# Kernel tuning notes

Hardware: AMD Instinct MI355X
Metric: run time of the kernel (lower is better)

The kernel has to match this reference:

```python
import jax, jax.numpy as jnp
import numpy as np

N_NODES = 6890
N_ANGLES = 8
K_CHEB = 15
N_DESC = 544
HIDDEN = 64
N_CLASS = 6890
M = N_ANGLES * N_NODES  # 55120, size of anisotropic Laplacian
DEG = 16
NNZ = M * DEG
BN_EPS = 1e-5


def setup_inputs() -> dict:
    key = jax.random.key(0)
    ks = jax.random.split(key, 16)
    x = jax.random.normal(ks[0], (N_NODES, N_DESC), dtype=jnp.float32)
    # sparse anisotropic Laplacian (M x M), ~DEG nnz per row
    rows = jnp.repeat(jnp.arange(M, dtype=jnp.int32), DEG)
    cols = jax.random.randint(ks[1], (NNZ,), 0, M, dtype=jnp.int32)
    vals = jax.random.normal(ks[2], (NNZ,), dtype=jnp.float32) * 0.1
    # conv1: (K, n_angles*n_desc, 64); conv2..6 stacked: (5, K, n_angles*64, 64)
    def xavier(k, shape, fan_in, fan_out):
        lim = np.sqrt(6.0 / (fan_in + fan_out))
        return jax.random.uniform(k, shape, jnp.float32, -lim, lim)
    W1 = xavier(ks[3], (K_CHEB, N_ANGLES * N_DESC, HIDDEN), N_ANGLES * N_DESC, HIDDEN)
    Wc = xavier(ks[4], (5, K_CHEB, N_ANGLES * HIDDEN, HIDDEN), N_ANGLES * HIDDEN, HIDDEN)
    conv_b = jnp.zeros((6, HIDDEN), jnp.float32)
    bn_gamma = jnp.ones((6, HIDDEN), jnp.float32)
    bn_beta = jnp.zeros((6, HIDDEN), jnp.float32)
    fc2_w = xavier(ks[5], (HIDDEN, 256), HIDDEN, 256)
    fc2_b = jnp.zeros((256,), jnp.float32)
    fc3_w = xavier(ks[6], (256, N_CLASS), 256, N_CLASS)
    fc3_b = jnp.zeros((N_CLASS,), jnp.float32)
    return {"x": x, "rows": rows, "cols": cols, "vals": vals,
            "W1": W1, "Wc": Wc, "conv_b": conv_b,
            "bn_gamma": bn_gamma, "bn_beta": bn_beta,
            "fc2_w": fc2_w, "fc2_b": fc2_b, "fc3_w": fc3_w, "fc3_b": fc3_b}


def _spmm(rows, cols, vals, T):
    # (M x M sparse) @ (M x C) via gather + segment-sum
    return jax.ops.segment_sum(vals[:, None] * T[cols], rows, num_segments=M)


def _acs_conv(x, rows, cols, vals, W, b):
    # x: (N, C). Chebyshev recurrence on the (A*N, C) angle-stacked signal.
    N, C = x.shape
    A = N_ANGLES

    def proj(T, Wk):
        # (A*N, C) -> (N, A*C) @ (A*C, out)
        return T.reshape(A, N, C).transpose(1, 0, 2).reshape(N, A * C) @ Wk

    T0 = jnp.tile(x, (A, 1))
    out = proj(T0, W[0])
    T1 = _spmm(rows, cols, vals, T0)
    out = out + proj(T1, W[1])
    for k in range(2, K_CHEB):
        T2 = 2.0 * _spmm(rows, cols, vals, T1) - T0
        out = out + proj(T2, W[k])
        T0, T1 = T1, T2
    return out + b


def _bn_relu(x, gamma, beta):
    # BatchNorm1d (training-mode batch stats, biased variance) + ReLU
    mean = jnp.mean(x, axis=0)
    var = jnp.var(x, axis=0)
    return jax.nn.relu((x - mean) * jax.lax.rsqrt(var + BN_EPS) * gamma + beta)


def reference(x, rows, cols, vals, W1, Wc, conv_b, bn_gamma, bn_beta,
              fc2_w, fc2_b, fc3_w, fc3_b):
    h = _bn_relu(_acs_conv(x, rows, cols, vals, W1, conv_b[0]), bn_gamma[0], bn_beta[0])
    for i in range(5):
        h = _bn_relu(_acs_conv(h, rows, cols, vals, Wc[i], conv_b[i + 1]),
                     bn_gamma[i + 1], bn_beta[i + 1])
    h = jax.nn.relu(h @ fc2_w + fc2_b)
    # dropout is identity at inference
    return h @ fc3_w + fc3_b
```

## Files before the change

kernel.cpp:

```cpp
#include <hip/hip_runtime.h>
#include <cstdint>
#include <cstddef>

#define NN 6890
#define NA 8
#define KC 15
#define ND 544
#define MR (NA * NN)
#define DEG 16
#define NNZ (MR * DEG)
#define BN_EPS 1e-5f
#define NRG 108
#define PB (NA * NRG)

typedef unsigned int u32;
typedef _Float16 f16;
typedef __attribute__((ext_vector_type(8))) _Float16 f16x8;
typedef __attribute__((ext_vector_type(4))) float f32x4;

union U4H8 { uint4 q; f16 h[8]; f16x8 v; };

__device__ __forceinline__ u32 packh(float a, float b) {
    union { f16 h[2]; u32 u; } c;
    c.h[0] = (f16)a; c.h[1] = (f16)b; return c.u;
}
__device__ __forceinline__ uint4 pack8h(const float* t) {
    uint4 m;
    m.x = packh(t[0], t[1]); m.y = packh(t[2], t[3]);
    m.z = packh(t[4], t[5]); m.w = packh(t[6], t[7]);
    return m;
}
__device__ __forceinline__ void acc8h(float* s, float v, uint4 g) {
    U4H8 c; c.q = g;
    #pragma unroll
    for (int i = 0; i < 8; ++i) s[i] += v * (float)c.h[i];
}

__global__ __launch_bounds__(256)
void prep_cv_kernel(const int* __restrict__ cols, const float* __restrict__ vals,
                    uint4* __restrict__ cvq)
{
    const int q = blockIdx.x * 256 + threadIdx.x;
    if (q >= NNZ / 4) return;
    const int4   c = ((const int4*)cols)[q];
    const float4 v = ((const float4*)vals)[q];
    uint4 o;
    o.x = ((u32)c.x & 0xffffu) | ((u32)c.y << 16);
    o.y = ((u32)c.z & 0xffffu) | ((u32)c.w << 16);
    o.z = packh(v.x, v.y);
    o.w = packh(v.z, v.w);
    cvq[q] = o;
}

template<int CC>
__global__ __launch_bounds__(256)
void tile_slab_kernel(const float* __restrict__ X, int C_in, int c0,
                      uint4* __restrict__ slab0)
{
    constexpr int LPR = CC / 8;
    constexpr int RPB = 256 / LPR;
    const int tid = threadIdx.x;
    const int j = tid % LPR, rloc = tid / LPR;
    const int r = blockIdx.x * RPB + rloc;
    if (r >= MR) return;
    const int n = r % NN;
    const float* xp = X + (size_t)n * C_in + c0 + 8 * j;
    const float4 t0 = *(const float4*)xp;
    const float4 t1 = *(const float4*)(xp + 4);
    float t[8] = { t0.x, t0.y, t0.z, t0.w, t1.x, t1.y, t1.z, t1.w };
    slab0[(size_t)r * LPR + j] = pack8h(t);
}

template<int CC, bool CHEB>
__device__ __forceinline__
void spmm_body(const uint4* __restrict__ sp, const uint4* __restrict__ sc,
               uint4* __restrict__ sw, const uint4* __restrict__ cvq)
{
    constexpr int LPR = CC / 8;
    constexpr int RPB = 256 / LPR;
    const int tid = threadIdx.x;
    const int j = tid % LPR, rloc = tid / LPR;
    const int r = blockIdx.x * RPB + rloc;
    if (r >= MR) return;

    int c[16]; float v[16];
    const uint4* cvp = cvq + (size_t)r * 4;
    #pragma unroll
    for (int q = 0; q < 4; ++q) {
        const uint4 cq = cvp[q];
        c[4 * q + 0] = cq.x & 0xffffu; c[4 * q + 1] = cq.x >> 16;
        c[4 * q + 2] = cq.y & 0xffffu; c[4 * q + 3] = cq.y >> 16;
        union { u32 u; f16 h[2]; } z, w_;
        z.u = cq.z; w_.u = cq.w;
        v[4 * q + 0] = (float)z.h[0]; v[4 * q + 1] = (float)z.h[1];
        v[4 * q + 2] = (float)w_.h[0]; v[4 * q + 3] = (float)w_.h[1];
    }
    float s[8] = {0.f, 0.f, 0.f, 0.f, 0.f, 0.f, 0.f, 0.f};
    #pragma unroll
    for (int d = 0; d < DEG; ++d)
        acc8h(s, v[d], sp[(size_t)c[d] * LPR + j]);
    float t[8];
    if (CHEB) {
        U4H8 p; p.q = sc[(size_t)r * LPR + j];
        #pragma unroll
        for (int i = 0; i < 8; ++i) t[i] = 2.f * s[i] - (float)p.h[i];
    } else {
        #pragma unroll
        for (int i = 0; i < 8; ++i) t[i] = s[i];
    }
    sw[(size_t)r * LPR + j] = pack8h(t);
}

template<int CC, bool FIRSTP>
__device__ __forceinline__
void proj_body(int pb, const uint4* __restrict__ sl, const float* __restrict__ W,
               float* __restrict__ part, int C_in, int c0, int kproj,
               u32* WH, u32* WL)
{
    constexpr int CCH = CC / 32;
    constexpr int LPR = CC / 8;
    const int tid = threadIdx.x;
    const int l = tid & 63, w = tid >> 6;
    const int a = pb / NRG, rg = pb % NRG;
    const int rows0 = rg * 64;
    const int hi16 = l >> 4;
    const float* Wk = W + ((size_t)kproj * NA * C_in + (size_t)a * C_in + c0) * 64;

    for (int e = tid; e < CCH * 1024; e += 256) {
        const int i2 = e & 3;
        const int ll = (e >> 2) & 63;
        const int nt = (e >> 8) & 3;
        const int h  = e >> 10;
        const int cc  = h * 32 + (ll >> 4) * 8 + 2 * i2;
        const int col = nt * 16 + (ll & 15);
        const float w0 = Wk[(size_t)cc * 64 + col];
        const float w1 = Wk[(size_t)(cc + 1) * 64 + col];
        const f16 h0 = (f16)w0, h1 = (f16)w1;
        union { f16 h[2]; u32 u; } ph, pl;
        ph.h[0] = h0; ph.h[1] = h1;
        pl.h[0] = (f16)(w0 - (float)h0); pl.h[1] = (f16)(w1 - (float)h1);
        WH[e] = ph.u; WL[e] = pl.u;
    }
    __syncthreads();

    const int arow = rows0 + w * 16 + (l & 15);
    const int arc  = arow < NN ? arow : NN - 1;
    const size_t abase = (size_t)(a * NN + arc) * LPR;

    f32x4 acc[4];
    #pragma unroll
    for (int nt = 0; nt < 4; ++nt) {
        #pragma unroll
        for (int rr = 0; rr < 4; ++rr) {
            const int orow = rows0 + w * 16 + hi16 * 4 + rr;
            float vv = 0.f;
            if (!FIRSTP && orow < NN)
                vv = part[((size_t)a * NN + orow) * 64 + nt * 16 + (l & 15)];
            acc[nt][rr] = vv;
        }
    }
    #pragma unroll
    for (int h = 0; h < CCH; ++h) {
        U4H8 af; af.q = sl[abase + h * 4 + hi16];
        #pragma unroll
        for (int nt = 0; nt < 4; ++nt) {
            const int be = ((h * 4 + nt) * 64 + l) * 4;
            U4H8 bh, bl;
            bh.q = *(const uint4*)&WH[be];
            bl.q = *(const uint4*)&WL[be];
            acc[nt] = __builtin_amdgcn_mfma_f32_16x16x32_f16(af.v, bh.v, acc[nt], 0, 0, 0);
            acc[nt] = __builtin_amdgcn_mfma_f32_16x16x32_f16(af.v, bl.v, acc[nt], 0, 0, 0);
        }
    }
    #pragma unroll
    for (int nt = 0; nt < 4; ++nt) {
        #pragma unroll
        for (int rr = 0; rr < 4; ++rr) {
            const int orow = rows0 + w * 16 + hi16 * 4 + rr;
            if (orow < NN)
                part[((size_t)a * NN + orow) * 64 + nt * 16 + (l & 15)] = acc[nt][rr];
        }
    }
}

template<int CC, bool CHEB, bool FIRSTP>
__global__ __launch_bounds__(256)
void step_kernel(const uint4* __restrict__ sp, const uint4* __restrict__ sc,
                 uint4* __restrict__ sw, const uint4* __restrict__ cvq,
                 const float* __restrict__ W, float* __restrict__ part,
                 int C_in, int c0, int kproj, int NB)
{
    constexpr int CCH = CC / 32;
    __shared__ u32 WH[CCH * 1024];
    __shared__ u32 WL[CCH * 1024];
    if ((int)blockIdx.x < NB)
        spmm_body<CC, CHEB>(sp, sc, sw, cvq);
    else
        proj_body<CC, FIRSTP>((int)blockIdx.x - NB, sp, W, part, C_in, c0, kproj, WH, WL);
}

template<int CC>
__global__ __launch_bounds__(256)
void proj_only_kernel(const uint4* __restrict__ sl, const float* __restrict__ W,
                      float* __restrict__ part, int C_in, int c0, int kproj)
{
    constexpr int CCH = CC / 32;
    __shared__ u32 WH[CCH * 1024];
    __shared__ u32 WL[CCH * 1024];
    proj_body<CC, false>((int)blockIdx.x, sl, W, part, C_in, c0, kproj, WH, WL);
}

__global__ void bn_reduce_kernel(const float* __restrict__ part, float* __restrict__ acc)
{
    const int e = blockIdx.x * blockDim.x + threadIdx.x;
    if (e >= NN * 64) return;
    float s = 0.f;
    #pragma unroll
    for (int a = 0; a < NA; ++a) s += part[(size_t)a * NN * 64 + e];
    acc[e] = s;
}

__global__ __launch_bounds__(256)
void bn_stats_kernel(const float* __restrict__ acc, const float* __restrict__ gamma,
                     const float* __restrict__ beta, float* __restrict__ bnp)
{
    const int h = blockIdx.x;
    float s = 0.f, sq = 0.f;
    for (int n = threadIdx.x; n < NN; n += 256) {
        const float v = acc[(size_t)n * 64 + h];
        s += v; sq += v * v;
    }
    __shared__ float ls[256], lq[256];
    ls[threadIdx.x] = s; lq[threadIdx.x] = sq;
    __syncthreads();
    for (int st = 128; st > 0; st >>= 1) {
        if (threadIdx.x < st) { ls[threadIdx.x] += ls[threadIdx.x + st]; lq[threadIdx.x] += lq[threadIdx.x + st]; }
        __syncthreads();
    }
    if (threadIdx.x == 0) {
        const float mean = ls[0] / (float)NN;
        const float var  = lq[0] / (float)NN - mean * mean;
        const float sc   = gamma[h] / sqrtf(var + BN_EPS);
        bnp[h]      = sc;
        bnp[64 + h] = beta[h] - mean * sc;
    }
}

__global__ void bn_apply_kernel(const float* __restrict__ acc, const float* __restrict__ bnp,
                                float* __restrict__ H)
{
    const int e = blockIdx.x * blockDim.x + threadIdx.x;
    if (e >= NN * 64) return;
    const int h = e & 63;
    const float v = acc[e] * bnp[h] + bnp[64 + h];
    H[e] = v > 0.f ? v : 0.f;
}

template<bool RELU>
__global__ __launch_bounds__(256)
void gemm_bias_kernel(const float* __restrict__ A, const float* __restrict__ B,
                      const float* __restrict__ bias, float* __restrict__ C,
                      int Mm, int Nn, int Kk)
{
    __shared__ float As[16][132];
    __shared__ float Bs[16][132];
    const int tx = threadIdx.x & 15, ty = threadIdx.x >> 4;
    const int m0 = blockIdx.y * 128, n0 = blockIdx.x * 128;
    const bool full = (m0 + 128 <= Mm) && (n0 + 128 <= Nn);
    float acc[8][8] = {};
    for (int k0 = 0; k0 < Kk; k0 += 16) {
        if (full) {
            #pragma unroll
            for (int e = threadIdx.x; e < 512; e += 256) {
                const int i = e >> 2, q = e & 3;
                const float4 a4 = *(const float4*)&A[(size_t)(m0 + i) * Kk + k0 + 4 * q];
                As[4 * q + 0][i] = a4.x; As[4 * q + 1][i] = a4.y;
                As[4 * q + 2][i] = a4.z; As[4 * q + 3][i] = a4.w;
            }
            #pragma unroll
            for (int e = threadIdx.x; e < 512; e += 256) {
                const int kk = e >> 5, q = e & 31;
                *(float4*)&Bs[kk][4 * q] = *(const float4*)&B[(size_t)(k0 + kk) * Nn + n0 + 4 * q];
            }
        } else {
            for (int e = threadIdx.x; e < 128 * 16; e += 256) {
                const int i = e >> 4, kk = e & 15;
                const int row = m0 + i;
                As[kk][i] = (row < Mm) ? A[(size_t)row * Kk + k0 + kk] : 0.f;
            }
            for (int e = threadIdx.x; e < 16 * 128; e += 256) {
                const int kk = e >> 7, jj = e & 127;
                const int col = n0 + jj;
                Bs[kk][jj] = (col < Nn) ? B[(size_t)(k0 + kk) * Nn + col] : 0.f;
            }
        }
        __syncthreads();
        #pragma unroll
        for (int kk = 0; kk < 16; ++kk) {
            float av[8], bv[8];
            *(float4*)&av[0] = *(const float4*)&As[kk][ty * 4];
            *(float4*)&av[4] = *(const float4*)&As[kk][64 + ty * 4];
            *(float4*)&bv[0] = *(const float4*)&Bs[kk][tx * 4];
            *(float4*)&bv[4] = *(const float4*)&Bs[kk][64 + tx * 4];
            #pragma unroll
            for (int i = 0; i < 8; ++i)
                #pragma unroll
                for (int jj = 0; jj < 8; ++jj)
                    acc[i][jj] += av[i] * bv[jj];
        }
        __syncthreads();
    }
    for (int i = 0; i < 8; ++i) {
        const int row = m0 + (i < 4 ? ty * 4 + i : 64 + ty * 4 + (i - 4));
        if (row >= Mm) continue;
        for (int jj = 0; jj < 8; ++jj) {
            const int col = n0 + (jj < 4 ? tx * 4 + jj : 64 + tx * 4 + (jj - 4));
            if (col >= Nn) continue;
            float v = acc[i][jj] + bias[col];
            if (RELU) v = fmaxf(v, 0.f);
            C[(size_t)row * Nn + col] = v;
        }
    }
}

__global__ __launch_bounds__(256)
void w3_split_kernel(const float* __restrict__ W, f16* __restrict__ Wh, f16* __restrict__ Wl)
{
    __shared__ float t[64][65];
    const int tid = threadIdx.x;
    const int n0 = blockIdx.x * 64, k0 = blockIdx.y * 64;
    for (int e = tid; e < 64 * 64; e += 256) {
        const int kk = e >> 6, nn = e & 63;
        const int gn = n0 + nn;
        t[kk][nn] = (gn < NN) ? W[(size_t)(k0 + kk) * NN + gn] : 0.f;
    }
    __syncthreads();
    for (int e = tid; e < 64 * 64; e += 256) {
        const int nn = e >> 6, kk = e & 63;
        const int gn = n0 + nn;
        if (gn < NN) {
            const float w = t[kk][nn];
            const f16 h = (f16)w;
            Wh[(size_t)gn * 256 + k0 + kk] = h;
            Wl[(size_t)gn * 256 + k0 + kk] = (f16)(w - (float)h);
        }
    }
}

__global__ __launch_bounds__(256)
void f2_split_kernel(const float* __restrict__ f2, f16* __restrict__ Ah, f16* __restrict__ Al)
{
    const int e = blockIdx.x * 256 + threadIdx.x;
    if (e >= NN * 256) return;
    const float v = f2[e];
    const f16 h = (f16)v;
    Ah[e] = h;
    Al[e] = (f16)(v - (float)h);
}

__global__ __launch_bounds__(256)
void fc3_mfma_kernel(const f16* __restrict__ Ah, const f16* __restrict__ Al,
                     const f16* __restrict__ Bh, const f16* __restrict__ Bl,
                     const float* __restrict__ bias, float* __restrict__ C)
{
    const int tid = threadIdx.x, l = tid & 63, w = tid >> 6;
    const int wm = w >> 1, wn = w & 1, hi16 = l >> 4;
    const int m0 = blockIdx.y * 128, n0 = blockIdx.x * 128;

    const f16* aph[4]; const f16* apl[4];
    const f16* bph[4]; const f16* bpl[4];
    #pragma unroll
    for (int mf = 0; mf < 4; ++mf) {
        int row = m0 + wm * 64 + mf * 16 + (l & 15);
        if (row > NN - 1) row = NN - 1;
        aph[mf] = Ah + (size_t)row * 256 + hi16 * 8;
        apl[mf] = Al + (size_t)row * 256 + hi16 * 8;
    }
    #pragma unroll
    for (int nf = 0; nf < 4; ++nf) {
        int col = n0 + wn * 64 + nf * 16 + (l & 15);
        if (col > NN - 1) col = NN - 1;
        bph[nf] = Bh + (size_t)col * 256 + hi16 * 8;
        bpl[nf] = Bl + (size_t)col * 256 + hi16 * 8;
    }

    f32x4 acc[4][4];
    #pragma unroll
    for (int mf = 0; mf < 4; ++mf)
        #pragma unroll
        for (int nf = 0; nf < 4; ++nf)
            acc[mf][nf] = (f32x4){0.f, 0.f, 0.f, 0.f};

    for (int k0 = 0; k0 < 256; k0 += 32) {
        f16x8 ah[4], al[4], bh[4], bl[4];
        #pragma unroll
        for (int mf = 0; mf < 4; ++mf) {
            ah[mf] = *(const f16x8*)(aph[mf] + k0);
            al[mf] = *(const f16x8*)(apl[mf] + k0);
        }
        #pragma unroll
        for (int nf = 0; nf < 4; ++nf) {
            bh[nf] = *(const f16x8*)(bph[nf] + k0);
            bl[nf] = *(const f16x8*)(bpl[nf] + k0);
        }
        #pragma unroll
        for (int mf = 0; mf < 4; ++mf)
            #pragma unroll
            for (int nf = 0; nf < 4; ++nf) {
                acc[mf][nf] = __builtin_amdgcn_mfma_f32_16x16x32_f16(ah[mf], bh[nf], acc[mf][nf], 0, 0, 0);
                acc[mf][nf] = __builtin_amdgcn_mfma_f32_16x16x32_f16(ah[mf], bl[nf], acc[mf][nf], 0, 0, 0);
                acc[mf][nf] = __builtin_amdgcn_mfma_f32_16x16x32_f16(al[mf], bh[nf], acc[mf][nf], 0, 0, 0);
            }
    }

    #pragma unroll
    for (int mf = 0; mf < 4; ++mf) {
        #pragma unroll
        for (int nf = 0; nf < 4; ++nf) {
            const int col = n0 + wn * 64 + nf * 16 + (l & 15);
            if (col >= NN) continue;
            const float bv = bias[col];
            #pragma unroll
            for (int rr = 0; rr < 4; ++rr) {
                const int row = m0 + wm * 64 + mf * 16 + hi16 * 4 + rr;
                if (row < NN)
                    C[(size_t)row * NN + col] = acc[mf][nf][rr] + bv;
            }
        }
    }
}

template<int CC>
static void run_chunk(bool first, const float* X, int C_in, int c0,
                      const uint4* cvq, const float* W,
                      uint4* const sl[3], float* part, hipStream_t stream)
{
    constexpr int RPB = 256 / (CC / 8);
    const int NB = (MR + RPB - 1) / RPB;

    tile_slab_kernel<CC><<<NB, 256, 0, stream>>>(X, C_in, c0, sl[0]);
    if (first)
        step_kernel<CC, false, true ><<<NB + PB, 256, 0, stream>>>(
            sl[0], sl[0], sl[1], cvq, W, part, C_in, c0, 0, NB);
    else
        step_kernel<CC, false, false><<<NB + PB, 256, 0, stream>>>(
            sl[0], sl[0], sl[1], cvq, W, part, C_in, c0, 0, NB);
    for (int k = 2; k < KC; ++k) {
        const int p = (k - 1) % 3, c = (k - 2) % 3, n = k % 3;
        step_kernel<CC, true, false><<<NB + PB, 256, 0, stream>>>(
            sl[p], sl[c], sl[n], cvq, W, part, C_in, c0, k - 1, NB);
    }
    proj_only_kernel<CC><<<PB, 256, 0, stream>>>(sl[(KC - 1) % 3], W, part, C_in, c0, KC - 1);
}

extern "C" void kernel_launch(void* const* d_in, const int* in_sizes, int n_in,
                              void* d_out, int out_size, void* d_ws, size_t ws_size,
                              hipStream_t stream)
{
    (void)in_sizes; (void)n_in; (void)out_size; (void)ws_size;
    const float* x     = (const float*)d_in[0];
    const int*   cols  = (const int*)  d_in[2];
    const float* vals  = (const float*)d_in[3];
    const float* W1    = (const float*)d_in[4];
    const float* Wc    = (const float*)d_in[5];
    const float* gamma = (const float*)d_in[7];
    const float* beta  = (const float*)d_in[8];
    const float* fc2w  = (const float*)d_in[9];
    const float* fc2b  = (const float*)d_in[10];
    const float* fc3w  = (const float*)d_in[11];
    const float* fc3b  = (const float*)d_in[12];

    const size_t MT   = (size_t)MR * 64;
    const size_t SLOT = (size_t)MR * 8;

    char* base = (char*)d_ws;
    size_t off = 0;
    uint4* cvq  = (uint4*)(base + off); off += (size_t)(NNZ / 4) * 16;
    uint4* slabs = (uint4*)(base + off); off += 3 * SLOT * 16;
    float* part = (float*)(base + off); off += MT * 4;
    float* acc  = (float*)(base + off); off += (size_t)NN * 64 * 4;
    float* H    = (float*)(base + off); off += (size_t)NN * 64 * 4;
    float* f2   = (float*)(base + off); off += (size_t)NN * 256 * 4;
    f16* f2h    = (f16*)(base + off);   off += (size_t)NN * 256 * 2;
    f16* f2l    = (f16*)(base + off);   off += (size_t)NN * 256 * 2;
    f16* W3h    = (f16*)(base + off);   off += (size_t)NN * 256 * 2;
    f16* W3l    = (f16*)(base + off);   off += (size_t)NN * 256 * 2;
    float* bnp  = (float*)(base + off);

    uint4* sl[3] = { slabs, slabs + SLOT, slabs + 2 * SLOT };

    prep_cv_kernel<<<(NNZ / 4 + 255) / 256, 256, 0, stream>>>(cols, vals, cvq);
    w3_split_kernel<<<dim3(108, 4), 256, 0, stream>>>(fc3w, W3h, W3l);

    for (int li = 0; li < 6; ++li) {
        const int C_in = (li == 0) ? ND : 64;
        const float* X = (li == 0) ? x : H;
        const float* W = (li == 0) ? W1 : Wc + (size_t)(li - 1) * KC * (NA * 64) * 64;
        const int nfull = C_in / 64;
        for (int c = 0; c < nfull; ++c)
            run_chunk<64>(c == 0, X, C_in, c * 64, cvq, W, sl, part, stream);
        if (C_in % 64)
            run_chunk<32>(false, X, C_in, nfull * 64, cvq, W, sl, part, stream);

        bn_reduce_kernel<<<(NN * 64 + 255) / 256, 256, 0, stream>>>(part, acc);
        bn_stats_kernel<<<64, 256, 0, stream>>>(acc, gamma + li * 64, beta + li * 64, bnp);
        bn_apply_kernel<<<(NN * 64 + 255) / 256, 256, 0, stream>>>(acc, bnp, H);
    }

    gemm_bias_kernel<true><<<dim3(2, 54), 256, 0, stream>>>(H, fc2w, fc2b, f2, NN, 256, 64);
    f2_split_kernel<<<(NN * 256 + 255) / 256, 256, 0, stream>>>(f2, f2h, f2l);
    fc3_mfma_kernel<<<dim3(54, 54), 256, 0, stream>>>(f2h, f2l, W3h, W3l, fc3b, (float*)d_out);
}
```

Measured before the change: 4.368 ms.

## Batch two Chebyshev projections per fused step and re-layout fc3 operands

Projection work is now done every other Chebyshev step, with each projection block handling two slabs and reusing the partial-sum read/write across both. A fourth slab buffer keeps the older slab alive, and odd steps launch SpMM-only kernels. The fc3 operands are also stored in a k-chunked [K/8][N][8] layout with vectorized split kernels, which should improve load coalescing. The cost is more workspace, an extra block-level barrier per projection block, and projection blocks that are twice as heavy on alternate launches, which may load-balance worse.

Measured after the change: 4.292 ms. No clear change (-1.7%).

```diff
diff --git a/kernel.cpp b/kernel.cpp
--- a/kernel.cpp
+++ b/kernel.cpp
@@ -111,11 +111,19 @@
     sw[(size_t)r * LPR + j] = pack8h(t);
 }
 
-template<int CC, bool FIRSTP>
+template<int CC, bool CHEB>
+__global__ __launch_bounds__(256)
+void spmm_only_kernel(const uint4* __restrict__ sp, const uint4* __restrict__ sc,
+                      uint4* __restrict__ sw, const uint4* __restrict__ cvq)
+{
+    spmm_body<CC, CHEB>(sp, sc, sw, cvq);
+}
+
+template<int CC, int NPROJ, bool FIRSTP>
 __device__ __forceinline__
-void proj_body(int pb, const uint4* __restrict__ sl, const float* __restrict__ W,
-               float* __restrict__ part, int C_in, int c0, int kproj,
-               u32* WH, u32* WL)
+void proj_body(int pb, const uint4* __restrict__ s0, const uint4* __restrict__ s1,
+               const float* __restrict__ W, float* __restrict__ part,
+               int C_in, int c0, int kbase, u32* WH, u32* WL)
 {
     constexpr int CCH = CC / 32;
     constexpr int LPR = CC / 8;
@@ -124,24 +132,6 @@
     const int a = pb / NRG, rg = pb % NRG;
     const int rows0 = rg * 64;
     const int hi16 = l >> 4;
-    const float* Wk = W + ((size_t)kproj * NA * C_in + (size_t)a * C_in + c0) * 64;
-
-    for (int e = tid; e < CCH * 1024; e += 256) {
-        const int i2 = e & 3;
-        const int ll = (e >> 2) & 63;
-        const int nt = (e >> 8) & 3;
-        const int h  = e >> 10;
-        const int cc  = h * 32 + (ll >> 4) * 8 + 2 * i2;
-        const int col = nt * 16 + (ll & 15);
-        const float w0 = Wk[(size_t)cc * 64 + col];
-        const float w1 = Wk[(size_t)(cc + 1) * 64 + col];
-        const f16 h0 = (f16)w0, h1 = (f16)w1;
-        union { f16 h[2]; u32 u; } ph, pl;
-        ph.h[0] = h0; ph.h[1] = h1;
-        pl.h[0] = (f16)(w0 - (float)h0); pl.h[1] = (f16)(w1 - (float)h1);
-        WH[e] = ph.u; WL[e] = pl.u;
-    }
-    __syncthreads();
 
     const int arow = rows0 + w * 16 + (l & 15);
     const int arc  = arow < NN ? arow : NN - 1;
@@ -159,19 +149,43 @@
             acc[nt][rr] = vv;
         }
     }
-    #pragma unroll
-    for (int h = 0; h < CCH; ++h) {
-        U4H8 af; af.q = sl[abase + h * 4 + hi16];
-        #pragma unroll
-        for (int nt = 0; nt < 4; ++nt) {
-            const int be = ((h * 4 + nt) * 64 + l) * 4;
-            U4H8 bh, bl;
-            bh.q = *(const uint4*)&WH[be];
-            bl.q = *(const uint4*)&WL[be];
-            acc[nt] = __builtin_amdgcn_mfma_f32_16x16x32_f16(af.v, bh.v, acc[nt], 0, 0, 0);
-            acc[nt] = __builtin_amdgcn_mfma_f32_16x16x32_f16(af.v, bl.v, acc[nt], 0, 0, 0);
-        }
-    }
+
+    #pragma unroll
+    for (int p = 0; p < NPROJ; ++p) {
+        const uint4* sl = (p == 0) ? s0 : s1;
+        const float* Wk = W + ((size_t)(kbase + p) * NA * C_in + (size_t)a * C_in + c0) * 64;
+        if (p) __syncthreads();
+        for (int e = tid; e < CCH * 1024; e += 256) {
+            const int i2 = e & 3;
+            const int ll = (e >> 2) & 63;
+            const int nt = (e >> 8) & 3;
+            const int h  = e >> 10;
+            const int cc  = h * 32 + (ll >> 4) * 8 + 2 * i2;
+            const int col = nt * 16 + (ll & 15);
+            const float w0 = Wk[(size_t)cc * 64 + col];
+            const float w1 = Wk[(size_t)(cc + 1) * 64 + col];
+            const f16 h0 = (f16)w0, h1 = (f16)w1;
+            union { f16 h[2]; u32 u; } ph, pl;
+            ph.h[0] = h0; ph.h[1] = h1;
+            pl.h[0] = (f16)(w0 - (float)h0); pl.h[1] = (f16)(w1 - (float)h1);
+            WH[e] = ph.u; WL[e] = pl.u;
+        }
+        __syncthreads();
+        #pragma unroll
+        for (int h = 0; h < CCH; ++h) {
+            U4H8 af; af.q = sl[abase + h * 4 + hi16];
+            #pragma unroll
+            for (int nt = 0; nt < 4; ++nt) {
+                const int be = ((h * 4 + nt) * 64 + l) * 4;
+                U4H8 bh, bl;
+                bh.q = *(const uint4*)&WH[be];
+                bl.q = *(const uint4*)&WL[be];
+                acc[nt] = __builtin_amdgcn_mfma_f32_16x16x32_f16(af.v, bh.v, acc[nt], 0, 0, 0);
+                acc[nt] = __builtin_amdgcn_mfma_f32_16x16x32_f16(af.v, bl.v, acc[nt], 0, 0, 0);
+            }
+        }
+    }
+
     #pragma unroll
     for (int nt = 0; nt < 4; ++nt) {
         #pragma unroll
@@ -183,31 +197,31 @@
     }
 }
 
-template<int CC, bool CHEB, bool FIRSTP>
-__global__ __launch_bounds__(256)
-void step_kernel(const uint4* __restrict__ sp, const uint4* __restrict__ sc,
-                 uint4* __restrict__ sw, const uint4* __restrict__ cvq,
-                 const float* __restrict__ W, float* __restrict__ part,
-                 int C_in, int c0, int kproj, int NB)
+template<int CC, bool FIRSTP>
+__global__ __launch_bounds__(256)
+void step2_kernel(const uint4* __restrict__ sp, const uint4* __restrict__ sc,
+                  uint4* __restrict__ sw, const uint4* __restrict__ cvq,
+                  const float* __restrict__ W, float* __restrict__ part,
+                  int C_in, int c0, int kbase, int NB)
 {
     constexpr int CCH = CC / 32;
     __shared__ u32 WH[CCH * 1024];
     __shared__ u32 WL[CCH * 1024];
     if ((int)blockIdx.x < NB)
-        spmm_body<CC, CHEB>(sp, sc, sw, cvq);
+        spmm_body<CC, true>(sp, sc, sw, cvq);
     else
-        proj_body<CC, FIRSTP>((int)blockIdx.x - NB, sp, W, part, C_in, c0, kproj, WH, WL);
+        proj_body<CC, 2, FIRSTP>((int)blockIdx.x - NB, sc, sp, W, part, C_in, c0, kbase, WH, WL);
 }
 
 template<int CC>
 __global__ __launch_bounds__(256)
-void proj_only_kernel(const uint4* __restrict__ sl, const float* __restrict__ W,
-                      float* __restrict__ part, int C_in, int c0, int kproj)
+void proj_final_kernel(const uint4* __restrict__ sl, const float* __restrict__ W,
+                       float* __restrict__ part, int C_in, int c0, int kproj)
 {
     constexpr int CCH = CC / 32;
     __shared__ u32 WH[CCH * 1024];
     __shared__ u32 WL[CCH * 1024];
-    proj_body<CC, false>((int)blockIdx.x, sl, W, part, C_in, c0, kproj, WH, WL);
+    proj_body<CC, 1, false>((int)blockIdx.x, sl, sl, W, part, C_in, c0, kproj, WH, WL);
 }
 
 __global__ void bn_reduce_kernel(const float* __restrict__ part, float* __restrict__ acc)
@@ -335,27 +349,41 @@
         t[kk][nn] = (gn < NN) ? W[(size_t)(k0 + kk) * NN + gn] : 0.f;
     }
     __syncthreads();
-    for (int e = tid; e < 64 * 64; e += 256) {
-        const int nn = e >> 6, kk = e & 63;
+    for (int e = tid; e < 64 * 8; e += 256) {
+        const int nn = e >> 3, c8 = e & 7;
         const int gn = n0 + nn;
-        if (gn < NN) {
-            const float w = t[kk][nn];
+        if (gn >= NN) continue;
+        const size_t ob = ((size_t)((k0 >> 3) + c8) * NN + gn) * 8;
+        f16 vh[8], vl[8];
+        #pragma unroll
+        for (int i = 0; i < 8; ++i) {
+            const float w = t[c8 * 8 + i][nn];
             const f16 h = (f16)w;
-            Wh[(size_t)gn * 256 + k0 + kk] = h;
-            Wl[(size_t)gn * 256 + k0 + kk] = (f16)(w - (float)h);
-        }
+            vh[i] = h; vl[i] = (f16)(w - (float)h);
+        }
+        *(uint4*)&Wh[ob] = *(const uint4*)vh;
+        *(uint4*)&Wl[ob] = *(const uint4*)vl;
     }
 }
 
 __global__ __launch_bounds__(256)
 void f2_split_kernel(const float* __restrict__ f2, f16* __restrict__ Ah, f16* __restrict__ Al)
 {
-    const int e = blockIdx.x * 256 + threadIdx.x;
-    if (e >= NN * 256) return;
-    const float v = f2[e];
-    const f16 h = (f16)v;
-    Ah[e] = h;
-    Al[e] = (f16)(v - (float)h);
+    const int row = blockIdx.x * 256 + threadIdx.x;
+    const int c = blockIdx.y;
+    if (row >= NN) return;
+    const float4 a0 = *(const float4*)&f2[(size_t)row * 256 + c * 8];
+    const float4 a1 = *(const float4*)&f2[(size_t)row * 256 + c * 8 + 4];
+    const float vv[8] = { a0.x, a0.y, a0.z, a0.w, a1.x, a1.y, a1.z, a1.w };
+    f16 vh[8], vl[8];
+    #pragma unroll
+    for (int i = 0; i < 8; ++i) {
+        const f16 h = (f16)vv[i];
+        vh[i] = h; vl[i] = (f16)(vv[i] - (float)h);
+    }
+    const size_t ob = ((size_t)c * NN + row) * 8;
+    *(uint4*)&Ah[ob] = *(const uint4*)vh;
+    *(uint4*)&Al[ob] = *(const uint4*)vl;
 }
 
 __global__ __launch_bounds__(256)
@@ -367,21 +395,18 @@
     const int wm = w >> 1, wn = w & 1, hi16 = l >> 4;
     const int m0 = blockIdx.y * 128, n0 = blockIdx.x * 128;
 
-    const f16* aph[4]; const f16* apl[4];
-    const f16* bph[4]; const f16* bpl[4];
+    size_t aoff[4], boff[4];
     #pragma unroll
     for (int mf = 0; mf < 4; ++mf) {
         int row = m0 + wm * 64 + mf * 16 + (l & 15);
         if (row > NN - 1) row = NN - 1;
-        aph[mf] = Ah + (size_t)row * 256 + hi16 * 8;
-        apl[mf] = Al + (size_t)row * 256 + hi16 * 8;
+        aoff[mf] = (size_t)row * 8;
     }
     #pragma unroll
     for (int nf = 0; nf < 4; ++nf) {
         int col = n0 + wn * 64 + nf * 16 + (l & 15);
         if (col > NN - 1) col = NN - 1;
-        bph[nf] = Bh + (size_t)col * 256 + hi16 * 8;
-        bpl[nf] = Bl + (size_t)col * 256 + hi16 * 8;
+        boff[nf] = (size_t)col * 8;
     }
 
     f32x4 acc[4][4];
@@ -392,16 +417,17 @@
             acc[mf][nf] = (f32x4){0.f, 0.f, 0.f, 0.f};
 
     for (int k0 = 0; k0 < 256; k0 += 32) {
+        const size_t cb = (size_t)((k0 >> 3) + hi16) * NN * 8;
         f16x8 ah[4], al[4], bh[4], bl[4];
         #pragma unroll
         for (int mf = 0; mf < 4; ++mf) {
-            ah[mf] = *(const f16x8*)(aph[mf] + k0);
-            al[mf] = *(const f16x8*)(apl[mf] + k0);
+            ah[mf] = *(const f16x8*)(Ah + cb + aoff[mf]);
+            al[mf] = *(const f16x8*)(Al + cb + aoff[mf]);
         }
         #pragma unroll
         for (int nf = 0; nf < 4; ++nf) {
-            bh[nf] = *(const f16x8*)(bph[nf] + k0);
-            bl[nf] = *(const f16x8*)(bpl[nf] + k0);
+            bh[nf] = *(const f16x8*)(Bh + cb + boff[nf]);
+            bl[nf] = *(const f16x8*)(Bl + cb + boff[nf]);
         }
         #pragma unroll
         for (int mf = 0; mf < 4; ++mf)
@@ -433,24 +459,27 @@
 template<int CC>
 static void run_chunk(bool first, const float* X, int C_in, int c0,
                       const uint4* cvq, const float* W,
-                      uint4* const sl[3], float* part, hipStream_t stream)
+                      uint4* const sl[4], float* part, hipStream_t stream)
 {
     constexpr int RPB = 256 / (CC / 8);
     const int NB = (MR + RPB - 1) / RPB;
 
     tile_slab_kernel<CC><<<NB, 256, 0, stream>>>(X, C_in, c0, sl[0]);
-    if (first)
-        step_kernel<CC, false, true ><<<NB + PB, 256, 0, stream>>>(
-            sl[0], sl[0], sl[1], cvq, W, part, C_in, c0, 0, NB);
-    else
-        step_kernel<CC, false, false><<<NB + PB, 256, 0, stream>>>(
-            sl[0], sl[0], sl[1], cvq, W, part, C_in, c0, 0, NB);
+    spmm_only_kernel<CC, false><<<NB, 256, 0, stream>>>(sl[0], sl[0], sl[1], cvq);
     for (int k = 2; k < KC; ++k) {
-        const int p = (k - 1) % 3, c = (k - 2) % 3, n = k % 3;
-        step_kernel<CC, true, false><<<NB + PB, 256, 0, stream>>>(
-            sl[p], sl[c], sl[n], cvq, W, part, C_in, c0, k - 1, NB);
-    }
-    proj_only_kernel<CC><<<PB, 256, 0, stream>>>(sl[(KC - 1) % 3], W, part, C_in, c0, KC - 1);
+        const int p = (k - 1) & 3, c = (k - 2) & 3, n = k & 3;
+        if (k & 1) {
+            spmm_only_kernel<CC, true><<<NB, 256, 0, stream>>>(sl[p], sl[c], sl[n], cvq);
+        } else {
+            if (first && k == 2)
+                step2_kernel<CC, true ><<<NB + PB, 256, 0, stream>>>(
+                    sl[p], sl[c], sl[n], cvq, W, part, C_in, c0, k - 2, NB);
+            else
+                step2_kernel<CC, false><<<NB + PB, 256, 0, stream>>>(
+                    sl[p], sl[c], sl[n], cvq, W, part, C_in, c0, k - 2, NB);
+        }
+    }
+    proj_final_kernel<CC><<<PB, 256, 0, stream>>>(sl[(KC - 1) & 3], W, part, C_in, c0, KC - 1);
 }
 
 extern "C" void kernel_launch(void* const* d_in, const int* in_sizes, int n_in,
@@ -476,7 +505,7 @@
     char* base = (char*)d_ws;
     size_t off = 0;
     uint4* cvq  = (uint4*)(base + off); off += (size_t)(NNZ / 4) * 16;
-    uint4* slabs = (uint4*)(base + off); off += 3 * SLOT * 16;
+    uint4* slabs = (uint4*)(base + off); off += 4 * SLOT * 16;
     float* part = (float*)(base + off); off += MT * 4;
     float* acc  = (float*)(base + off); off += (size_t)NN * 64 * 4;
     float* H    = (float*)(base + off); off += (size_t)NN * 64 * 4;
@@ -487,7 +516,7 @@
     f16* W3l    = (f16*)(base + off);   off += (size_t)NN * 256 * 2;
     float* bnp  = (float*)(base + off);
 
-    uint4* sl[3] = { slabs, slabs + SLOT, slabs + 2 * SLOT };
+    uint4* sl[4] = { slabs, slabs + SLOT, slabs + 2 * SLOT, slabs + 3 * SLOT };
 
     prep_cv_kernel<<<(NNZ / 4 + 255) / 256, 256, 0, stream>>>(cols, vals, cvq);
     w3_split_kernel<<<dim3(108, 4), 256, 0, stream>>>(fc3w, W3h, W3l);
@@ -508,6 +537,6 @@
     }
 
     gemm_bias_kernel<true><<<dim3(2, 54), 256, 0, stream>>>(H, fc2w, fc2b, f2, NN, 256, 64);
-    f2_split_kernel<<<(NN * 256 + 255) / 256, 256, 0, stream>>>(f2, f2h, f2l);
+    f2_split_kernel<<<dim3(27, 32), 256, 0, stream>>>(f2, f2h, f2l);
     fc3_mfma_kernel<<<dim3(54, 54), 256, 0, stream>>>(f2h, f2l, W3h, W3l, fc3b, (float*)d_out);
 }
```
